# Kernel optimization log

Measured on AMD Instinct MI355X. Metric: run time of the kernel, lower is better.

## Reference

```python
import jax, jax.numpy as jnp
import numpy as np


def setup_inputs() -> dict:
    key = jax.random.key(0)
    ks = jax.random.split(key, 11)
    N, K, M = 2, 2048, 1024   # batch, seq_len, d_model (dim_in)
    H, D = 16, 64             # num_heads, dim_out (per-head q/k/v dim)
    s_in = 1.0 / np.sqrt(M)
    s_out = 1.0 / np.sqrt(H * D)
    return {
        "query": jax.random.normal(ks[0], (N, K, M), jnp.float32),
        "key":   jax.random.normal(ks[1], (N, K, M), jnp.float32),
        "value": jax.random.normal(ks[2], (N, K, M), jnp.float32),
        "Wq": jax.random.normal(ks[3], (H, D, M), jnp.float32) * s_in,
        "bq": jax.random.normal(ks[4], (H, D), jnp.float32) * 0.01,
        "Wk": jax.random.normal(ks[5], (H, D, M), jnp.float32) * s_in,
        "bk": jax.random.normal(ks[6], (H, D), jnp.float32) * 0.01,
        "Wv": jax.random.normal(ks[7], (H, D, M), jnp.float32) * s_in,
        "bv": jax.random.normal(ks[8], (H, D), jnp.float32) * 0.01,
        "Wo": jax.random.normal(ks[9], (M, H * D), jnp.float32) * s_out,
        "bo": jax.random.normal(ks[10], (M,), jnp.float32) * 0.01,
    }


def reference(query, key, value, Wq, bq, Wk, bk, Wv, bv, Wo, bo):
    # Batched over heads instead of the original python loop; same math.
    # q,k: [H,N,K,D], v: [H,N,K,D]
    q = jnp.einsum('nkm,hdm->hnkd', query, Wq) + bq[:, None, None, :]
    k = jnp.einsum('nkm,hdm->hnkd', key,   Wk) + bk[:, None, None, :]
    v = jnp.einsum('nkm,hdm->hnkd', value, Wv) + bv[:, None, None, :]
    D = q.shape[-1]
    # scaled_dot_product scales by sqrt of the projected dim (dim_out)
    scores = jnp.einsum('hnkd,hnld->hnkl', q, k) / jnp.sqrt(jnp.asarray(D, q.dtype))
    attn = jax.nn.softmax(scores, axis=-1)            # [H,N,K,K]
    y = jnp.einsum('hnkl,hnld->hnkd', attn, v)        # [H,N,K,D]
    H, N, K, _ = y.shape
    # concat heads along feature dim: [N,K,H*D]
    y_cat = jnp.transpose(y, (1, 2, 0, 3)).reshape(N, K, H * D)
    return y_cat @ Wo.T + bo
```

## Files before the change

kernel.cpp:

```cpp
#include <hip/hip_runtime.h>
#include <hip/hip_bf16.h>

#define NB 2
#define SEQ 2048
#define DM 1024
#define NH 16
#define HD 64

typedef unsigned short u16;
typedef unsigned int u32;
typedef __attribute__((ext_vector_type(8))) short bf16x8;
typedef __attribute__((ext_vector_type(4))) float f32x4;
typedef __attribute__((ext_vector_type(4))) unsigned short u16x4;
typedef __attribute__((ext_vector_type(2))) unsigned int u32x2;

#define MFMA __builtin_amdgcn_mfma_f32_16x16x32_bf16

#define QSCALE 0.18033688011112042f

__device__ __forceinline__ u16 bf16_rne(float x) {
    unsigned int u = __float_as_uint(x);
    return (u16)((u + 0x7FFFu + ((u >> 16) & 1u)) >> 16);
}
__device__ __forceinline__ float bf16f(u16 h) {
    return __uint_as_float(((unsigned int)h) << 16);
}
__device__ __forceinline__ void split2(float x, u16& h, u16& l) {
    h = bf16_rne(x);
    l = bf16_rne(x - bf16f(h));
}
__device__ __forceinline__ u32 cvt_pk_bf16(float lo, float hi) {
    u32 r;
    asm("v_cvt_pk_bf16_f32 %0, %1, %2" : "=v"(r) : "v"(lo), "v"(hi));
    return r;
}
__device__ __forceinline__ float exp2_fast(float x) {
#if __has_builtin(__builtin_amdgcn_exp2f)
    return __builtin_amdgcn_exp2f(x);
#else
    float r;
    asm("v_exp_f32 %0, %1" : "=v"(r) : "v"(x));
    return r;
#endif
}

__device__ __forceinline__ void async16(const u16* g, u16* l) {
    typedef const __attribute__((address_space(1))) u32* GP;
    typedef __attribute__((address_space(3))) u32* LP;
    __builtin_amdgcn_global_load_lds((GP)g, (LP)l, 16, 0, 0);
}

__global__ __launch_bounds__(256) void presplit(
    const float* __restrict__ x0, const float* __restrict__ x1,
    const float* __restrict__ x2, const float* __restrict__ wq,
    const float* __restrict__ wk, const float* __restrict__ wv,
    const float* __restrict__ wo,
    u16* __restrict__ xh, u16* __restrict__ wh, u16* __restrict__ wl)
{
    const int seg = blockIdx.y;
    const float* src;
    u16* dh;
    u16* dl = nullptr;
    int n4;
    float sc = 1.f;
    if (seg < 3) {
        src = (seg == 0) ? x0 : (seg == 1) ? x1 : x2;
        dh = xh + (size_t)seg * 4194304;
        n4 = 1048576;
    } else {
        int s2 = seg - 3;
        src = (s2 == 0) ? wq : (s2 == 1) ? wk : (s2 == 2) ? wv : wo;
        dh = wh + (size_t)s2 * 1048576;
        if (s2 == 3) dl = wl + (size_t)s2 * 1048576;
        n4 = 262144;
        if (s2 == 0) sc = QSCALE;
    }
    for (int i = blockIdx.x * 256 + threadIdx.x; i < n4; i += gridDim.x * 256) {
        float4 v = ((const float4*)src)[i];
        v.x *= sc; v.y *= sc; v.z *= sc; v.w *= sc;
        u16 h0 = bf16_rne(v.x), h1 = bf16_rne(v.y);
        u16 h2 = bf16_rne(v.z), h3 = bf16_rne(v.w);
        u16x4 hv = {h0, h1, h2, h3};
        *(u16x4*)(dh + (size_t)i * 4) = hv;
        if (dl) {
            u16x4 lv = {bf16_rne(v.x - bf16f(h0)), bf16_rne(v.y - bf16f(h1)),
                        bf16_rne(v.z - bf16f(h2)), bf16_rne(v.w - bf16f(h3))};
            *(u16x4*)(dl + (size_t)i * 4) = lv;
        }
    }
}

__global__ __launch_bounds__(256, 4) void gemm_qkv(
    const u16* __restrict__ xh3, const u16* __restrict__ wh3,
    const float* __restrict__ bq, const float* __restrict__ bk,
    const float* __restrict__ bv,
    u16* qh, u16* ql, u16* kh, u16* vth)
{
    __shared__ u16 A0[128][32], A1[128][32], B0[128][32], B1[128][32];

    const int tid = threadIdx.x, lane = tid & 63, w = tid >> 6;
    const int lg = lane >> 4, lc = lane & 15;

    const int id = blockIdx.x + 8 * blockIdx.y;
    const int swz = (id & 7) * 32 + (id >> 3);
    const int c0 = (swz & 7) * 128, r0 = (swz >> 3) * 128;

    const int z = blockIdx.z;
    const u16* ag = xh3 + (size_t)z * 4194304;
    const u16* bg = wh3 + (size_t)z * 1048576;
    const float* bias = (z == 0) ? bq : (z == 1) ? bk : bv;

    const u16* gb = (w < 2) ? ag : bg;
    u16* lb = (w == 0) ? &A0[0][0] : (w == 1) ? &A1[0][0]
            : (w == 2) ? &B0[0][0] : &B1[0][0];
    const int rbase = (w < 2) ? r0 : c0;
    const int colofs = (w & 1) * 32;
    const u16* gsrc0 = gb + (size_t)(rbase + (lane >> 2)) * DM + colofs + (lane & 3) * 8;

    const int wr = (w >> 1) * 64, wc = (w & 1) * 64;

    f32x4 acc[4][4];
#pragma unroll
    for (int i = 0; i < 4; ++i)
#pragma unroll
        for (int j = 0; j < 4; ++j) acc[i][j] = (f32x4)0.f;

    for (int ks = 0; ks < DM; ks += 64) {
        __syncthreads();
#pragma unroll
        for (int i = 0; i < 8; ++i)
            async16(gsrc0 + (size_t)i * 16 * DM + ks, lb + i * 512);
        __syncthreads();

#pragma unroll
        for (int kk = 0; kk < 2; ++kk) {
            const u16(*Ak)[32] = kk ? A1 : A0;
            const u16(*Bk)[32] = kk ? B1 : B0;
            bf16x8 ah[4], bh[4];
#pragma unroll
            for (int rt = 0; rt < 4; ++rt)
                ah[rt] = *(const bf16x8*)&Ak[wr + rt * 16 + lc][lg * 8];
#pragma unroll
            for (int jt = 0; jt < 4; ++jt)
                bh[jt] = *(const bf16x8*)&Bk[wc + jt * 16 + lc][lg * 8];
#pragma unroll
            for (int jt = 0; jt < 4; ++jt)
#pragma unroll
                for (int rt = 0; rt < 4; ++rt)
                    acc[rt][jt] = MFMA(ah[rt], bh[jt], acc[rt][jt], 0, 0, 0);
        }
    }

#pragma unroll
    for (int rt = 0; rt < 4; ++rt)
#pragma unroll
        for (int jt = 0; jt < 4; ++jt)
#pragma unroll
            for (int r = 0; r < 4; ++r) {
                int row = r0 + wr + rt * 16 + lg * 4 + r;
                int col = c0 + wc + jt * 16 + lc;
                int h = col >> 6, d = col & 63, n = row >> 11, s = row & 2047;
                if (z == 0) {
                    float v = acc[rt][jt][r] + bias[col] * QSCALE;
                    size_t idx = ((size_t)((h << 1) | n) * SEQ + s) * HD + d;
                    u16 hh, ll; split2(v, hh, ll);
                    qh[idx] = hh; ql[idx] = ll;
                } else if (z == 1) {
                    float v = acc[rt][jt][r] + bias[col];
                    size_t idx = ((size_t)((h << 1) | n) * SEQ + s) * HD + d;
                    kh[idx] = bf16_rne(v);
                } else {
                    float v = acc[rt][jt][r] + bias[col];
                    size_t idx = ((size_t)((h << 1) | n) * HD + d) * SEQ + s;
                    vth[idx] = bf16_rne(v);
                }
            }
}

__global__ __launch_bounds__(256, 2) void gemm_proj(
    const u16* __restrict__ yh, const u16* __restrict__ yl,
    const u16* __restrict__ woh, const u16* __restrict__ wol,
    const float* __restrict__ bo, float* __restrict__ outf)
{
    __shared__ u16 Ah[128][32], Al[128][32], Bh[128][32], Bl[128][32];

    const int tid = threadIdx.x, lane = tid & 63, w = tid >> 6;
    const int lg = lane >> 4, lc = lane & 15;

    const int id = blockIdx.x + 8 * blockIdx.y;
    const int swz = (id & 7) * 32 + (id >> 3);
    const int c0 = (swz & 7) * 128, r0 = (swz >> 3) * 128;

    const u16* gb = (w == 0) ? yh : (w == 1) ? yl : (w == 2) ? woh : wol;
    u16* lb = (w == 0) ? &Ah[0][0] : (w == 1) ? &Al[0][0] : (w == 2) ? &Bh[0][0] : &Bl[0][0];
    const int rbase = (w < 2) ? r0 : c0;
    const u16* gsrc0 = gb + (size_t)(rbase + (lane >> 2)) * DM + (lane & 3) * 8;

    const int wr = (w >> 1) * 64, wc = (w & 1) * 64;

    f32x4 acc[4][4];
#pragma unroll
    for (int i = 0; i < 4; ++i)
#pragma unroll
        for (int j = 0; j < 4; ++j) acc[i][j] = (f32x4)0.f;

    for (int ks = 0; ks < DM; ks += 32) {
        __syncthreads();
#pragma unroll
        for (int i = 0; i < 8; ++i)
            async16(gsrc0 + (size_t)i * 16 * DM + ks, lb + i * 512);
        __syncthreads();

        bf16x8 ah[4], al[4];
#pragma unroll
        for (int rt = 0; rt < 4; ++rt) {
            ah[rt] = *(const bf16x8*)&Ah[wr + rt * 16 + lc][lg * 8];
            al[rt] = *(const bf16x8*)&Al[wr + rt * 16 + lc][lg * 8];
        }
#pragma unroll
        for (int jt = 0; jt < 4; ++jt) {
            bf16x8 bh2 = *(const bf16x8*)&Bh[wc + jt * 16 + lc][lg * 8];
            bf16x8 bl2 = *(const bf16x8*)&Bl[wc + jt * 16 + lc][lg * 8];
#pragma unroll
            for (int rt = 0; rt < 4; ++rt) {
                acc[rt][jt] = MFMA(ah[rt], bh2, acc[rt][jt], 0, 0, 0);
                acc[rt][jt] = MFMA(ah[rt], bl2, acc[rt][jt], 0, 0, 0);
                acc[rt][jt] = MFMA(al[rt], bh2, acc[rt][jt], 0, 0, 0);
            }
        }
    }

#pragma unroll
    for (int rt = 0; rt < 4; ++rt)
#pragma unroll
        for (int jt = 0; jt < 4; ++jt)
#pragma unroll
            for (int r = 0; r < 4; ++r) {
                int row = r0 + wr + rt * 16 + lg * 4 + r;
                int col = c0 + wc + jt * 16 + lc;
                outf[(size_t)row * DM + col] = acc[rt][jt][r] + bo[col];
            }
}

__global__ __launch_bounds__(256, 4) void attn_k(
    const u16* __restrict__ qh, const u16* __restrict__ ql,
    const u16* __restrict__ kh, const u16* __restrict__ vth,
    u16* __restrict__ yh, u16* __restrict__ yl)
{
    __shared__ u16 Ks[64][72], Vs[64][72];
    __shared__ u16 Pb[4][32][72];

    const int tid = threadIdx.x, lane = tid & 63, w = tid >> 6;
    const int lg = lane >> 4, lc = lane & 15;

    const int id = blockIdx.x + 16 * blockIdx.y;
    const int widx = (id & 7) * 64 + (id >> 3);
    const int hn = widx >> 4;
    const int qb0 = (widx & 15) * 128;

    bf16x8 qfh[2][2], qfl[2][2];
    const size_t qkbase = (size_t)hn * SEQ * HD;
#pragma unroll
    for (int rt = 0; rt < 2; ++rt)
#pragma unroll
        for (int kc = 0; kc < 2; ++kc) {
            size_t off = qkbase + (size_t)(qb0 + w * 32 + rt * 16 + lc) * HD + kc * 32 + lg * 8;
            qfh[rt][kc] = *(const bf16x8*)(qh + off);
            qfl[rt][kc] = *(const bf16x8*)(ql + off);
        }

    f32x4 ot[2][4];
#pragma unroll
    for (int i = 0; i < 2; ++i)
#pragma unroll
        for (int j = 0; j < 4; ++j) ot[i][j] = (f32x4)0.f;
    float m_[2] = {-3e38f, -3e38f};
    float s_[2] = {0.f, 0.f};

    const size_t vbase = (size_t)hn * HD * SEQ;

    for (int kt = 0; kt < SEQ; kt += 64) {
        __syncthreads();
#pragma unroll
        for (int i = 0; i < 2; ++i) {
            int f = tid + 256 * i, row = f >> 3, kb = (f & 7) * 8;
            size_t ksrc = qkbase + (size_t)(kt + row) * HD + kb;
            *(bf16x8*)&Ks[row][kb] = *(const bf16x8*)(kh + ksrc);
            size_t vsrc = vbase + (size_t)row * SEQ + kt + kb;
            *(bf16x8*)&Vs[row][kb] = *(const bf16x8*)(vth + vsrc);
        }
        __syncthreads();

        f32x4 st[2][4];
#pragma unroll
        for (int i = 0; i < 2; ++i)
#pragma unroll
            for (int j = 0; j < 4; ++j) st[i][j] = (f32x4)0.f;
        __builtin_amdgcn_s_setprio(1);
#pragma unroll
        for (int jt = 0; jt < 4; ++jt)
#pragma unroll
            for (int kc = 0; kc < 2; ++kc) {
                bf16x8 k8 = *(const bf16x8*)&Ks[jt * 16 + lc][kc * 32 + lg * 8];
#pragma unroll
                for (int rt = 0; rt < 2; ++rt) {
                    st[rt][jt] = MFMA(k8, qfh[rt][kc], st[rt][jt], 0, 0, 0);
                    st[rt][jt] = MFMA(k8, qfl[rt][kc], st[rt][jt], 0, 0, 0);
                }
            }
        __builtin_amdgcn_s_setprio(0);

#pragma unroll
        for (int rt = 0; rt < 2; ++rt) {
            float t0 = fmaxf(fmaxf(st[rt][0][0], st[rt][0][1]),
                             fmaxf(st[rt][0][2], st[rt][0][3]));
            float t1 = fmaxf(fmaxf(st[rt][1][0], st[rt][1][1]),
                             fmaxf(st[rt][1][2], st[rt][1][3]));
            float t2 = fmaxf(fmaxf(st[rt][2][0], st[rt][2][1]),
                             fmaxf(st[rt][2][2], st[rt][2][3]));
            float t3 = fmaxf(fmaxf(st[rt][3][0], st[rt][3][1]),
                             fmaxf(st[rt][3][2], st[rt][3][3]));
            float t = fmaxf(fmaxf(t0, t1), fmaxf(t2, t3));
            t = fmaxf(t, __shfl_xor(t, 16));
            t = fmaxf(t, __shfl_xor(t, 32));
            if (__any(t - m_[rt] > 8.0f)) {
                float mnew = fmaxf(m_[rt], t);
                float resc = exp2_fast(m_[rt] - mnew);
                m_[rt] = mnew;
                s_[rt] *= resc;
#pragma unroll
                for (int dt = 0; dt < 4; ++dt) {
                    ot[rt][dt][0] *= resc; ot[rt][dt][1] *= resc;
                    ot[rt][dt][2] *= resc; ot[rt][dt][3] *= resc;
                }
            }
            const float mm = m_[rt];
#pragma unroll
            for (int jt = 0; jt < 4; ++jt) {
                float p0 = exp2_fast(st[rt][jt][0] - mm);
                float p1 = exp2_fast(st[rt][jt][1] - mm);
                float p2 = exp2_fast(st[rt][jt][2] - mm);
                float p3 = exp2_fast(st[rt][jt][3] - mm);
                s_[rt] += (p0 + p1) + (p2 + p3);
                u32x2 pk = {cvt_pk_bf16(p0, p1), cvt_pk_bf16(p2, p3)};
                *(u32x2*)&Pb[w][rt * 16 + lc][jt * 16 + lg * 4] = pk;
            }
        }

        bf16x8 pb[2][2];
#pragma unroll
        for (int rt = 0; rt < 2; ++rt)
#pragma unroll
            for (int jc = 0; jc < 2; ++jc)
                pb[rt][jc] = *(const bf16x8*)&Pb[w][rt * 16 + lc][jc * 32 + lg * 8];
        __builtin_amdgcn_s_setprio(1);
#pragma unroll
        for (int dt = 0; dt < 4; ++dt)
#pragma unroll
            for (int jc = 0; jc < 2; ++jc) {
                bf16x8 v8 = *(const bf16x8*)&Vs[dt * 16 + lc][jc * 32 + lg * 8];
#pragma unroll
                for (int rt = 0; rt < 2; ++rt)
                    ot[rt][dt] = MFMA(v8, pb[rt][jc], ot[rt][dt], 0, 0, 0);
            }
        __builtin_amdgcn_s_setprio(0);
    }

    const int h = hn >> 1, n = hn & 1;
#pragma unroll
    for (int rt = 0; rt < 2; ++rt) {
        float v = s_[rt];
        v += __shfl_xor(v, 16);
        v += __shfl_xor(v, 32);
        s_[rt] = 1.f / v;
    }
#pragma unroll
    for (int rt = 0; rt < 2; ++rt) {
        const int srow = qb0 + w * 32 + rt * 16 + lc;
        size_t rowoff = (size_t)(n * SEQ + srow) * DM + h * HD;
#pragma unroll
        for (int dt = 0; dt < 4; ++dt) {
            u16x4 hv, lv;
#pragma unroll
            for (int r = 0; r < 4; ++r) {
                float y = ot[rt][dt][r] * s_[rt];
                u16 hh, ll; split2(y, hh, ll);
                hv[r] = hh; lv[r] = ll;
            }
            size_t idx = rowoff + dt * 16 + lg * 4;
            *(u16x4*)(yh + idx) = hv;
            *(u16x4*)(yl + idx) = lv;
        }
    }
}

extern "C" void kernel_launch(void* const* d_in, const int* in_sizes, int n_in,
                              void* d_out, int out_size, void* d_ws, size_t ws_size,
                              hipStream_t stream)
{
    const float* query = (const float*)d_in[0];
    const float* key_  = (const float*)d_in[1];
    const float* value = (const float*)d_in[2];
    const float* Wq = (const float*)d_in[3];
    const float* bq = (const float*)d_in[4];
    const float* Wk = (const float*)d_in[5];
    const float* bk = (const float*)d_in[6];
    const float* Wv = (const float*)d_in[7];
    const float* bv = (const float*)d_in[8];
    const float* Wo = (const float*)d_in[9];
    const float* bo = (const float*)d_in[10];
    float* out = (float*)d_out;

    char* p = (char*)d_ws;
    u16* wh  = (u16*)(p);
    u16* wl  = (u16*)(p + 8388608ull);
    u16* qh  = (u16*)(p + 16777216ull);
    u16* ql  = (u16*)(p + 25165824ull);
    u16* kh  = (u16*)(p + 33554432ull);
    u16* vth = (u16*)(p + 50331648ull);
    u16* xh  = (u16*)(p + 67108864ull);
    u16* yh  = (u16*)(p + 67108864ull);
    u16* yl  = (u16*)(p + 75497472ull);

    presplit<<<dim3(256, 7), 256, 0, stream>>>(
        query, key_, value, Wq, Wk, Wv, Wo, xh, wh, wl);

    gemm_qkv<<<dim3(8, 32, 3), 256, 0, stream>>>(
        xh, wh, bq, bk, bv, qh, ql, kh, vth);

    attn_k<<<dim3(16, 32), 256, 0, stream>>>(qh, ql, kh, vth, yh, yl);

    gemm_proj<<<dim3(8, 32), 256, 0, stream>>>(
        yh, yl, wh + 3145728ull, wl + 3145728ull, bo, out);
}
```

Measured before the change: 280.6 us.

## Double-buffer K/V with async LDS loads, swizzle LDS, halve query tile per block

Restructures the attention kernel so K/V tiles are loaded asynchronously straight into LDS into a double buffer. The next tile's load overlaps the current tile's MFMA and softmax work. LDS layouts for K, V and P are XOR-swizzled in place of padding to avoid bank conflicts, and each block now covers 64 query rows instead of 128, doubling the grid. The trade-off is that each K/V tile is reloaded by twice as many blocks, in exchange for more parallelism and less load latency exposed per iteration.

```diff
diff --git a/kernel.cpp b/kernel.cpp
--- a/kernel.cpp
+++ b/kernel.cpp
@@ -247,151 +247,147 @@
     const u16* __restrict__ kh, const u16* __restrict__ vth,
     u16* __restrict__ yh, u16* __restrict__ yl)
 {
-    __shared__ u16 Ks[64][72], Vs[64][72];
-    __shared__ u16 Pb[4][32][72];
+    __shared__ u16 Ks[2][64][64], Vs[2][64][64];
+    __shared__ u16 Pb[4][16][64];
 
     const int tid = threadIdx.x, lane = tid & 63, w = tid >> 6;
     const int lg = lane >> 4, lc = lane & 15;
 
-    const int id = blockIdx.x + 16 * blockIdx.y;
-    const int widx = (id & 7) * 64 + (id >> 3);
-    const int hn = widx >> 4;
-    const int qb0 = (widx & 15) * 128;
-
-    bf16x8 qfh[2][2], qfl[2][2];
+    const int id = blockIdx.x + 32 * blockIdx.y;
+    const int widx = (id & 7) * 128 + (id >> 3);
+    const int hn = widx >> 5;
+    const int qb0 = (widx & 31) * 64;
+
     const size_t qkbase = (size_t)hn * SEQ * HD;
-#pragma unroll
-    for (int rt = 0; rt < 2; ++rt)
-#pragma unroll
-        for (int kc = 0; kc < 2; ++kc) {
-            size_t off = qkbase + (size_t)(qb0 + w * 32 + rt * 16 + lc) * HD + kc * 32 + lg * 8;
-            qfh[rt][kc] = *(const bf16x8*)(qh + off);
-            qfl[rt][kc] = *(const bf16x8*)(ql + off);
-        }
-
-    f32x4 ot[2][4];
-#pragma unroll
-    for (int i = 0; i < 2; ++i)
-#pragma unroll
-        for (int j = 0; j < 4; ++j) ot[i][j] = (f32x4)0.f;
-    float m_[2] = {-3e38f, -3e38f};
-    float s_[2] = {0.f, 0.f};
-
     const size_t vbase = (size_t)hn * HD * SEQ;
 
-    for (int kt = 0; kt < SEQ; kt += 64) {
+    const int srow = lane >> 3;
+    const int sg = (lane & 7) ^ (srow & 7);
+
+#define STAGE_KV(buf, kt0)                                                   \
+    {                                                                        \
+        _Pragma("unroll")                                                    \
+        for (int cc = 0; cc < 2; ++cc) {                                     \
+            const int c = w * 2 + cc;                                        \
+            const int r = c * 8 + srow;                                      \
+            async16(kh + qkbase + (size_t)((kt0) + r) * HD + sg * 8,         \
+                    &Ks[buf][0][0] + c * 512);                               \
+            async16(vth + vbase + (size_t)r * SEQ + (kt0) + sg * 8,          \
+                    &Vs[buf][0][0] + c * 512);                               \
+        }                                                                    \
+    }
+
+    bf16x8 qfh[2], qfl[2];
+#pragma unroll
+    for (int kc = 0; kc < 2; ++kc) {
+        size_t off = qkbase + (size_t)(qb0 + w * 16 + lc) * HD + kc * 32 + lg * 8;
+        qfh[kc] = *(const bf16x8*)(qh + off);
+        qfl[kc] = *(const bf16x8*)(ql + off);
+    }
+
+    f32x4 ot[4];
+#pragma unroll
+    for (int j = 0; j < 4; ++j) ot[j] = (f32x4)0.f;
+    float m_ = -3e38f, s_ = 0.f;
+
+    STAGE_KV(0, 0);
+    asm volatile("s_waitcnt vmcnt(0)" ::: "memory");
+    __syncthreads();
+
+    int cur = 0;
+    for (int t = 0; t < SEQ / 64; ++t) {
+        if (t < SEQ / 64 - 1) STAGE_KV(cur ^ 1, (t + 1) * 64);
+
+        f32x4 st[4];
+#pragma unroll
+        for (int j = 0; j < 4; ++j) st[j] = (f32x4)0.f;
+        __builtin_amdgcn_s_setprio(1);
+#pragma unroll
+        for (int jt = 0; jt < 4; ++jt)
+#pragma unroll
+            for (int kc = 0; kc < 2; ++kc) {
+                bf16x8 k8 = *(const bf16x8*)
+                    &Ks[cur][jt * 16 + lc][(((kc << 2) | lg) ^ (lc & 7)) * 8];
+                st[jt] = MFMA(k8, qfh[kc], st[jt], 0, 0, 0);
+                st[jt] = MFMA(k8, qfl[kc], st[jt], 0, 0, 0);
+            }
+        __builtin_amdgcn_s_setprio(0);
+
+        {
+            float t0 = fmaxf(fmaxf(st[0][0], st[0][1]), fmaxf(st[0][2], st[0][3]));
+            float t1 = fmaxf(fmaxf(st[1][0], st[1][1]), fmaxf(st[1][2], st[1][3]));
+            float t2 = fmaxf(fmaxf(st[2][0], st[2][1]), fmaxf(st[2][2], st[2][3]));
+            float t3 = fmaxf(fmaxf(st[3][0], st[3][1]), fmaxf(st[3][2], st[3][3]));
+            float tm = fmaxf(fmaxf(t0, t1), fmaxf(t2, t3));
+            tm = fmaxf(tm, __shfl_xor(tm, 16));
+            tm = fmaxf(tm, __shfl_xor(tm, 32));
+            if (__any(tm - m_ > 8.0f)) {
+                float mnew = fmaxf(m_, tm);
+                float resc = exp2_fast(m_ - mnew);
+                m_ = mnew;
+                s_ *= resc;
+#pragma unroll
+                for (int dt = 0; dt < 4; ++dt) {
+                    ot[dt][0] *= resc; ot[dt][1] *= resc;
+                    ot[dt][2] *= resc; ot[dt][3] *= resc;
+                }
+            }
+#pragma unroll
+            for (int jt = 0; jt < 4; ++jt) {
+                float p0 = exp2_fast(st[jt][0] - m_);
+                float p1 = exp2_fast(st[jt][1] - m_);
+                float p2 = exp2_fast(st[jt][2] - m_);
+                float p3 = exp2_fast(st[jt][3] - m_);
+                s_ += (p0 + p1) + (p2 + p3);
+                u32x2 pk = {cvt_pk_bf16(p0, p1), cvt_pk_bf16(p2, p3)};
+                *(u32x2*)&Pb[w][lc][(jt * 16 + lg * 4) ^ ((lc & 7) << 3)] = pk;
+            }
+        }
+
+        bf16x8 pb[2];
+#pragma unroll
+        for (int jc = 0; jc < 2; ++jc)
+            pb[jc] = *(const bf16x8*)
+                &Pb[w][lc][(jc * 32 + lg * 8) ^ ((lc & 7) << 3)];
+        __builtin_amdgcn_s_setprio(1);
+#pragma unroll
+        for (int dt = 0; dt < 4; ++dt)
+#pragma unroll
+            for (int jc = 0; jc < 2; ++jc) {
+                bf16x8 v8 = *(const bf16x8*)
+                    &Vs[cur][dt * 16 + lc][(((jc << 2) | lg) ^ (lc & 7)) * 8];
+                ot[dt] = MFMA(v8, pb[jc], ot[dt], 0, 0, 0);
+            }
+        __builtin_amdgcn_s_setprio(0);
+
+        asm volatile("s_waitcnt vmcnt(0)" ::: "memory");
         __syncthreads();
-#pragma unroll
-        for (int i = 0; i < 2; ++i) {
-            int f = tid + 256 * i, row = f >> 3, kb = (f & 7) * 8;
-            size_t ksrc = qkbase + (size_t)(kt + row) * HD + kb;
-            *(bf16x8*)&Ks[row][kb] = *(const bf16x8*)(kh + ksrc);
-            size_t vsrc = vbase + (size_t)row * SEQ + kt + kb;
-            *(bf16x8*)&Vs[row][kb] = *(const bf16x8*)(vth + vsrc);
-        }
-        __syncthreads();
-
-        f32x4 st[2][4];
-#pragma unroll
-        for (int i = 0; i < 2; ++i)
-#pragma unroll
-            for (int j = 0; j < 4; ++j) st[i][j] = (f32x4)0.f;
-        __builtin_amdgcn_s_setprio(1);
-#pragma unroll
-        for (int jt = 0; jt < 4; ++jt)
-#pragma unroll
-            for (int kc = 0; kc < 2; ++kc) {
-                bf16x8 k8 = *(const bf16x8*)&Ks[jt * 16 + lc][kc * 32 + lg * 8];
-#pragma unroll
-                for (int rt = 0; rt < 2; ++rt) {
-                    st[rt][jt] = MFMA(k8, qfh[rt][kc], st[rt][jt], 0, 0, 0);
-                    st[rt][jt] = MFMA(k8, qfl[rt][kc], st[rt][jt], 0, 0, 0);
-                }
-            }
-        __builtin_amdgcn_s_setprio(0);
-
-#pragma unroll
-        for (int rt = 0; rt < 2; ++rt) {
-            float t0 = fmaxf(fmaxf(st[rt][0][0], st[rt][0][1]),
-                             fmaxf(st[rt][0][2], st[rt][0][3]));
-            float t1 = fmaxf(fmaxf(st[rt][1][0], st[rt][1][1]),
-                             fmaxf(st[rt][1][2], st[rt][1][3]));
-            float t2 = fmaxf(fmaxf(st[rt][2][0], st[rt][2][1]),
-                             fmaxf(st[rt][2][2], st[rt][2][3]));
-            float t3 = fmaxf(fmaxf(st[rt][3][0], st[rt][3][1]),
-                             fmaxf(st[rt][3][2], st[rt][3][3]));
-            float t = fmaxf(fmaxf(t0, t1), fmaxf(t2, t3));
-            t = fmaxf(t, __shfl_xor(t, 16));
-            t = fmaxf(t, __shfl_xor(t, 32));
-            if (__any(t - m_[rt] > 8.0f)) {
-                float mnew = fmaxf(m_[rt], t);
-                float resc = exp2_fast(m_[rt] - mnew);
-                m_[rt] = mnew;
-                s_[rt] *= resc;
-#pragma unroll
-                for (int dt = 0; dt < 4; ++dt) {
-                    ot[rt][dt][0] *= resc; ot[rt][dt][1] *= resc;
-                    ot[rt][dt][2] *= resc; ot[rt][dt][3] *= resc;
-                }
-            }
-            const float mm = m_[rt];
-#pragma unroll
-            for (int jt = 0; jt < 4; ++jt) {
-                float p0 = exp2_fast(st[rt][jt][0] - mm);
-                float p1 = exp2_fast(st[rt][jt][1] - mm);
-                float p2 = exp2_fast(st[rt][jt][2] - mm);
-                float p3 = exp2_fast(st[rt][jt][3] - mm);
-                s_[rt] += (p0 + p1) + (p2 + p3);
-                u32x2 pk = {cvt_pk_bf16(p0, p1), cvt_pk_bf16(p2, p3)};
-                *(u32x2*)&Pb[w][rt * 16 + lc][jt * 16 + lg * 4] = pk;
-            }
-        }
-
-        bf16x8 pb[2][2];
-#pragma unroll
-        for (int rt = 0; rt < 2; ++rt)
-#pragma unroll
-            for (int jc = 0; jc < 2; ++jc)
-                pb[rt][jc] = *(const bf16x8*)&Pb[w][rt * 16 + lc][jc * 32 + lg * 8];
-        __builtin_amdgcn_s_setprio(1);
-#pragma unroll
-        for (int dt = 0; dt < 4; ++dt)
-#pragma unroll
-            for (int jc = 0; jc < 2; ++jc) {
-                bf16x8 v8 = *(const bf16x8*)&Vs[dt * 16 + lc][jc * 32 + lg * 8];
-#pragma unroll
-                for (int rt = 0; rt < 2; ++rt)
-                    ot[rt][dt] = MFMA(v8, pb[rt][jc], ot[rt][dt], 0, 0, 0);
-            }
-        __builtin_amdgcn_s_setprio(0);
+        cur ^= 1;
     }
 
     const int h = hn >> 1, n = hn & 1;
-#pragma unroll
-    for (int rt = 0; rt < 2; ++rt) {
-        float v = s_[rt];
+    {
+        float v = s_;
         v += __shfl_xor(v, 16);
         v += __shfl_xor(v, 32);
-        s_[rt] = 1.f / v;
-    }
-#pragma unroll
-    for (int rt = 0; rt < 2; ++rt) {
-        const int srow = qb0 + w * 32 + rt * 16 + lc;
-        size_t rowoff = (size_t)(n * SEQ + srow) * DM + h * HD;
-#pragma unroll
-        for (int dt = 0; dt < 4; ++dt) {
-            u16x4 hv, lv;
-#pragma unroll
-            for (int r = 0; r < 4; ++r) {
-                float y = ot[rt][dt][r] * s_[rt];
-                u16 hh, ll; split2(y, hh, ll);
-                hv[r] = hh; lv[r] = ll;
-            }
-            size_t idx = rowoff + dt * 16 + lg * 4;
-            *(u16x4*)(yh + idx) = hv;
-            *(u16x4*)(yl + idx) = lv;
-        }
-    }
+        s_ = 1.f / v;
+    }
+    const int qrow = qb0 + w * 16 + lc;
+    size_t rowoff = (size_t)(n * SEQ + qrow) * DM + h * HD;
+#pragma unroll
+    for (int dt = 0; dt < 4; ++dt) {
+        u16x4 hv, lv;
+#pragma unroll
+        for (int r = 0; r < 4; ++r) {
+            float y = ot[dt][r] * s_;
+            u16 hh, ll; split2(y, hh, ll);
+            hv[r] = hh; lv[r] = ll;
+        }
+        size_t idx = rowoff + dt * 16 + lg * 4;
+        *(u16x4*)(yh + idx) = hv;
+        *(u16x4*)(yl + idx) = lv;
+    }
+#undef STAGE_KV
 }
 
 extern "C" void kernel_launch(void* const* d_in, const int* in_sizes, int n_in,
@@ -428,7 +424,7 @@
     gemm_qkv<<<dim3(8, 32, 3), 256, 0, stream>>>(
         xh, wh, bq, bk, bv, qh, ql, kh, vth);
 
-    attn_k<<<dim3(16, 32), 256, 0, stream>>>(qh, ql, kh, vth, yh, yl);
+    attn_k<<<dim3(32, 32), 256, 0, stream>>>(qh, ql, kh, vth, yh, yl);
 
     gemm_proj<<<dim3(8, 32), 256, 0, stream>>>(
         yh, yl, wh + 3145728ull, wl + 3145728ull, bo, out);
```

Measured after the change: 284.0 us. About the same (+1.2%).
